# Optimization experiments

Hardware: AMD Instinct MI355X
Metric: run time of the kernel (lower is better)

## Reference

```python
import jax, jax.numpy as jnp
import numpy as np

N_NODES = 100000
N_EDGES = 640000
IN_CH = 128
OUT_CH = 128


def setup_inputs() -> dict:
    key = jax.random.key(0)
    k1, k2, k3, k4, k5, k6 = jax.random.split(key, 6)
    row = jax.random.randint(k1, (N_EDGES,), 0, N_NODES, dtype=jnp.int64 if jax.config.jax_enable_x64 else jnp.int32)
    col = jax.random.randint(k2, (N_EDGES,), 0, N_NODES, dtype=jnp.int64 if jax.config.jax_enable_x64 else jnp.int32)
    vals = jax.random.uniform(k3, (N_EDGES,), dtype=jnp.float32)
    X = jax.random.normal(k4, (N_NODES, IN_CH), dtype=jnp.float32)
    weights = jax.random.normal(k5, (IN_CH, OUT_CH), dtype=jnp.float32)
    bias = jax.random.normal(k6, (OUT_CH,), dtype=jnp.float32)
    return {"row": row, "col": col, "vals": vals, "X": X, "weights": weights, "bias": bias}


def reference(row, col, vals, X, weights, bias):
    # A is sparse COO: A[row[e], col[e]] = vals[e]
    N = X.shape[0]
    # dense feature transform: [N, out]
    XTheta = X @ weights
    # D = (row_sum(A) + 1)^(-1/2)
    deg = jax.ops.segment_sum(vals, row, num_segments=N)
    D = jax.lax.rsqrt(deg + 1.0)
    # Xprime = D * (A @ (D * XTheta))
    Y = D[:, None] * XTheta                                    # [N, out]
    msgs = vals[:, None] * Y[col]                              # [E, out] gather
    AY = jax.ops.segment_sum(msgs, row, num_segments=N)        # [N, out] scatter-add
    return D[:, None] * AY + bias
```

## Files before the change

kernel.cpp:

```cpp
#include <hip/hip_runtime.h>
#include <hip/hip_bf16.h>


#define N_CH 128
#define WT_LD 136

typedef __attribute__((ext_vector_type(8))) short short8;
typedef __attribute__((ext_vector_type(4))) float f32x4;
typedef __attribute__((ext_vector_type(4))) unsigned short ushort4v;

__device__ inline unsigned short f2bf(float f) {
    unsigned u = __float_as_uint(f);
    return (unsigned short)((u + 0x7FFFu + ((u >> 16) & 1u)) >> 16);
}
__device__ inline float bf2f(unsigned short h) {
    return __uint_as_float(((unsigned)h) << 16);
}

__global__ __launch_bounds__(256) void rank_kernel(const int* __restrict__ row,
                                                   int* __restrict__ cnt,
                                                   int* __restrict__ rank, int E) {
    int e0 = blockIdx.x * 2048 + threadIdx.x;
#pragma unroll
    for (int j = 0; j < 8; ++j) {
        int e = e0 + j * 256;
        if (e < E) rank[e] = atomicAdd(&cnt[row[e]], 1);
    }
}

__global__ __launch_bounds__(256) void scan1_kernel(const int* __restrict__ cnt,
                                                    int* __restrict__ pos,
                                                    int* __restrict__ bsum, int N) {
    __shared__ int s[256];
    int t = threadIdx.x;
    int i = blockIdx.x * 256 + t;
    int v = (i < N) ? cnt[i] : 0;
    s[t] = v;
    __syncthreads();
    for (int off = 1; off < 256; off <<= 1) {
        int x = (t >= off) ? s[t - off] : 0;
        __syncthreads();
        s[t] += x;
        __syncthreads();
    }
    if (i < N) pos[i] = s[t] - v;
    if (t == 255) bsum[blockIdx.x] = s[t];
}

__global__ __launch_bounds__(512) void scan2_kernel(int* __restrict__ bsum, int nb) {
    __shared__ int s[512];
    int t = threadIdx.x;
    int v = (t < nb) ? bsum[t] : 0;
    s[t] = v;
    __syncthreads();
    for (int off = 1; off < 512; off <<= 1) {
        int x = (t >= off) ? s[t - off] : 0;
        __syncthreads();
        s[t] += x;
        __syncthreads();
    }
    if (t < nb) bsum[t] = s[t] - v;
}

__global__ __launch_bounds__(256) void scan3_kernel(int* __restrict__ pos,
                                                    const int* __restrict__ bsum, int N) {
    int i = blockIdx.x * 256 + threadIdx.x;
    if (i < N) pos[i] += bsum[blockIdx.x];
}

__global__ __launch_bounds__(256) void place_kernel(const int* __restrict__ row,
                                                    const int* __restrict__ col,
                                                    const float* __restrict__ vals,
                                                    const int* __restrict__ pos,
                                                    const int* __restrict__ rank,
                                                    uint2* __restrict__ epack, int E) {
    int e0 = blockIdx.x * 1024 + threadIdx.x;
#pragma unroll
    for (int j = 0; j < 4; ++j) {
        int e = e0 + j * 256;
        if (e < E) {
            int r = row[e];
            int p = pos[r] + rank[e];
            epack[p] = make_uint2((unsigned)col[e], __float_as_uint(vals[e]));
        }
    }
}

__global__ __launch_bounds__(256) void dinv_kernel(const int* __restrict__ pos,
                                                   const uint2* __restrict__ epack,
                                                   float* __restrict__ dinv, int N, int E) {
    int n = blockIdx.x * 256 + threadIdx.x;
    if (n >= N) return;
    int start = pos[n];
    int end = (n + 1 < N) ? pos[n + 1] : E;
    float s = 0.f;
    for (int e = start; e < end; ++e) s += __uint_as_float(epack[e].y);
    dinv[n] = rsqrtf(s + 1.0f);
}

__global__ __launch_bounds__(256) void wcvt_kernel(const float* __restrict__ W,
                                                   unsigned short* __restrict__ Wt) {
    int i = blockIdx.x * 256 + threadIdx.x;
    int k = i >> 7, n = i & 127;
    Wt[n * N_CH + k] = f2bf(W[k * N_CH + n]);
}

__global__ __launch_bounds__(256) void gemm_kernel(const float* __restrict__ X,
                                                   const unsigned short* __restrict__ Wt,
                                                   const float* __restrict__ dinv,
                                                   unsigned short* __restrict__ Ybf, int N) {
    __shared__ unsigned short Wl[N_CH * WT_LD];

    const int t = threadIdx.x;
    const short8* Wg = (const short8*)Wt;
#pragma unroll
    for (int j = 0; j < 8; ++j) {
        int idx = t + 256 * j;
        int r = idx >> 4, cc = idx & 15;
        *(short8*)(Wl + r * WT_LD + cc * 8) = Wg[idx];
    }
    __syncthreads();

    const int lane = t & 63;
    const int wv = t >> 6;
    const int m = lane & 15;
    const int q = lane >> 4;

#pragma unroll
    for (int i = 0; i < 2; ++i) {
        const int base = (blockIdx.x * 8 + wv * 2 + i) * 16;
        if (base >= N) break;

        short8 a[4];
        const float* xrow = X + (size_t)(base + m) * N_CH + q * 8;
#pragma unroll
        for (int c = 0; c < 4; ++c) {
            f32x4 lo = *(const f32x4*)(xrow + c * 32);
            f32x4 hi = *(const f32x4*)(xrow + c * 32 + 4);
            short8 v;
            v[0] = (short)f2bf(lo[0]); v[1] = (short)f2bf(lo[1]);
            v[2] = (short)f2bf(lo[2]); v[3] = (short)f2bf(lo[3]);
            v[4] = (short)f2bf(hi[0]); v[5] = (short)f2bf(hi[1]);
            v[6] = (short)f2bf(hi[2]); v[7] = (short)f2bf(hi[3]);
            a[c] = v;
        }

        f32x4 acc[8];
#pragma unroll
        for (int tt = 0; tt < 8; ++tt) acc[tt] = (f32x4){0.f, 0.f, 0.f, 0.f};

#pragma unroll
        for (int tt = 0; tt < 8; ++tt) {
            const unsigned short* wrow = Wl + (tt * 16 + m) * WT_LD + q * 8;
#pragma unroll
            for (int c = 0; c < 4; ++c) {
                short8 b = *(const short8*)(wrow + c * 32);
                acc[tt] = __builtin_amdgcn_mfma_f32_16x16x32_bf16(a[c], b, acc[tt], 0, 0, 0);
            }
        }

        float ds[4];
#pragma unroll
        for (int r = 0; r < 4; ++r) ds[r] = dinv[base + q * 4 + r];

#pragma unroll
        for (int tt = 0; tt < 8; ++tt) {
#pragma unroll
            for (int r = 0; r < 4; ++r) {
                Ybf[(size_t)(base + q * 4 + r) * N_CH + tt * 16 + m] = f2bf(acc[tt][r] * ds[r]);
            }
        }
    }
}

__global__ __launch_bounds__(256) void gather_kernel(const int* __restrict__ pos,
                                                     const uint2* __restrict__ epack,
                                                     const unsigned short* __restrict__ Ybf,
                                                     const float* __restrict__ dinv,
                                                     const float* __restrict__ bias,
                                                     float* __restrict__ out, int N, int E) {
    unsigned gid = blockIdx.x * 256u + threadIdx.x;
    int n = gid >> 5;
    if (n >= N) return;
    int lane = gid & 31;
    int c = lane * 4;

    int e = pos[n];
    int end = (n + 1 < N) ? pos[n + 1] : E;

    float4 acc = make_float4(0.f, 0.f, 0.f, 0.f);
    for (; e + 4 <= end; e += 4) {
        uint2 p0 = epack[e + 0];
        uint2 p1 = epack[e + 1];
        uint2 p2 = epack[e + 2];
        uint2 p3 = epack[e + 3];
        ushort4v y0 = *(const ushort4v*)(Ybf + (size_t)p0.x * N_CH + c);
        ushort4v y1 = *(const ushort4v*)(Ybf + (size_t)p1.x * N_CH + c);
        ushort4v y2 = *(const ushort4v*)(Ybf + (size_t)p2.x * N_CH + c);
        ushort4v y3 = *(const ushort4v*)(Ybf + (size_t)p3.x * N_CH + c);
        float v0 = __uint_as_float(p0.y);
        float v1 = __uint_as_float(p1.y);
        float v2 = __uint_as_float(p2.y);
        float v3 = __uint_as_float(p3.y);
        acc.x += v0 * bf2f(y0[0]) + v1 * bf2f(y1[0]) + v2 * bf2f(y2[0]) + v3 * bf2f(y3[0]);
        acc.y += v0 * bf2f(y0[1]) + v1 * bf2f(y1[1]) + v2 * bf2f(y2[1]) + v3 * bf2f(y3[1]);
        acc.z += v0 * bf2f(y0[2]) + v1 * bf2f(y1[2]) + v2 * bf2f(y2[2]) + v3 * bf2f(y3[2]);
        acc.w += v0 * bf2f(y0[3]) + v1 * bf2f(y1[3]) + v2 * bf2f(y2[3]) + v3 * bf2f(y3[3]);
    }
    for (; e < end; ++e) {
        uint2 p = epack[e];
        float v = __uint_as_float(p.y);
        ushort4v y = *(const ushort4v*)(Ybf + (size_t)p.x * N_CH + c);
        acc.x += v * bf2f(y[0]);
        acc.y += v * bf2f(y[1]);
        acc.z += v * bf2f(y[2]);
        acc.w += v * bf2f(y[3]);
    }

    float d = dinv[n];
    float4 b = ((const float4*)bias)[lane];
    float4 o;
    o.x = acc.x * d + b.x;
    o.y = acc.y * d + b.y;
    o.z = acc.z * d + b.z;
    o.w = acc.w * d + b.w;
    ((float4*)(out + (size_t)n * N_CH))[lane] = o;
}

extern "C" void kernel_launch(void* const* d_in, const int* in_sizes, int n_in,
                              void* d_out, int out_size, void* d_ws, size_t ws_size,
                              hipStream_t stream) {
    const int*   row  = (const int*)d_in[0];
    const int*   col  = (const int*)d_in[1];
    const float* vals = (const float*)d_in[2];
    const float* X    = (const float*)d_in[3];
    const float* W    = (const float*)d_in[4];
    const float* bias = (const float*)d_in[5];
    float* out = (float*)d_out;

    const int E = in_sizes[0];
    const int N = in_sizes[3] / N_CH;
    const int nb = (N + 255) / 256;

    uint2*          epack = (uint2*)d_ws;
    unsigned short* Ybf   = (unsigned short*)(epack + E);
    float*          dinv  = (float*)(Ybf + (size_t)N * N_CH);
    int*            cnt   = (int*)(dinv + N);
    int*            pos   = cnt + N;
    int*            rank  = pos + N;
    int*            bsum  = rank + E;
    unsigned short* Wt    = (unsigned short*)(bsum + nb);

    hipMemsetAsync(cnt, 0, (size_t)N * sizeof(int), stream);

    rank_kernel<<<(E + 2047) / 2048, 256, 0, stream>>>(row, cnt, rank, E);
    scan1_kernel<<<nb, 256, 0, stream>>>(cnt, pos, bsum, N);
    scan2_kernel<<<1, 512, 0, stream>>>(bsum, nb);
    scan3_kernel<<<nb, 256, 0, stream>>>(pos, bsum, N);
    place_kernel<<<(E + 1023) / 1024, 256, 0, stream>>>(row, col, vals, pos, rank, epack, E);
    dinv_kernel<<<nb, 256, 0, stream>>>(pos, epack, dinv, N, E);

    wcvt_kernel<<<64, 256, 0, stream>>>(W, Wt);
    int tiles = (N + 15) / 16;
    int gblocks = (tiles + 7) / 8;
    gemm_kernel<<<gblocks, 256, 0, stream>>>(X, Wt, dinv, Ybf, N);

    unsigned gth = (unsigned)N * 32u;
    gather_kernel<<<(gth + 255) / 256, 256, 0, stream>>>(pos, epack, Ybf, dinv, bias, out, N, E);
}
```

Measured before the change: 215.0 us.

## Merge preprocessing kernels: fuse degree atomics, scan passes, and gemm with edge placement

Degree accumulation moves into the rank kernel as float atomics, and the W conversion runs as extra blocks of that same launch. The scan2/scan3 pair is replaced by one kernel in which each block sums the preceding block totals itself and also computes dinv. The GEMM and edge-placement kernels are fused into a single launch split by block index. This cuts the launch count from about nine to five and removes the pass that re-reads edges to build dinv. In exchange it adds float atomics, which make the degree sum order nondeterministic, and a scan whose per-block cost grows with the block index.

Result: slower. 237.0 us (+10.3%).

```diff
diff --git a/kernel.cpp b/kernel.cpp
--- a/kernel.cpp
+++ b/kernel.cpp
@@ -18,13 +18,28 @@
 }
 
 __global__ __launch_bounds__(256) void rank_kernel(const int* __restrict__ row,
+                                                   const float* __restrict__ vals,
                                                    int* __restrict__ cnt,
-                                                   int* __restrict__ rank, int E) {
+                                                   float* __restrict__ deg,
+                                                   int* __restrict__ rank,
+                                                   const float* __restrict__ W,
+                                                   unsigned short* __restrict__ Wt,
+                                                   int E, int rankBlocks) {
+    if ((int)blockIdx.x >= rankBlocks) {
+        int i = (blockIdx.x - rankBlocks) * 256 + threadIdx.x;
+        int k = i >> 7, n = i & 127;
+        Wt[n * N_CH + k] = f2bf(W[k * N_CH + n]);
+        return;
+    }
     int e0 = blockIdx.x * 2048 + threadIdx.x;
 #pragma unroll
     for (int j = 0; j < 8; ++j) {
         int e = e0 + j * 256;
-        if (e < E) rank[e] = atomicAdd(&cnt[row[e]], 1);
+        if (e < E) {
+            int r = row[e];
+            rank[e] = atomicAdd(&cnt[r], 1);
+            atomicAdd(&deg[r], vals[e]);
+        }
     }
 }
 
@@ -47,69 +62,50 @@
     if (t == 255) bsum[blockIdx.x] = s[t];
 }
 
-__global__ __launch_bounds__(512) void scan2_kernel(int* __restrict__ bsum, int nb) {
-    __shared__ int s[512];
+__global__ __launch_bounds__(256) void scan3_kernel(int* __restrict__ pos,
+                                                    const int* __restrict__ bsum,
+                                                    const float* __restrict__ deg,
+                                                    float* __restrict__ dinv, int N) {
+    __shared__ int s[256];
     int t = threadIdx.x;
-    int v = (t < nb) ? bsum[t] : 0;
-    s[t] = v;
+    int b = blockIdx.x;
+    int acc = 0;
+    for (int j = t; j < b; j += 256) acc += bsum[j];
+    s[t] = acc;
     __syncthreads();
-    for (int off = 1; off < 512; off <<= 1) {
-        int x = (t >= off) ? s[t - off] : 0;
+    for (int off = 128; off > 0; off >>= 1) {
+        if (t < off) s[t] += s[t + off];
         __syncthreads();
-        s[t] += x;
-        __syncthreads();
-    }
-    if (t < nb) bsum[t] = s[t] - v;
-}
-
-__global__ __launch_bounds__(256) void scan3_kernel(int* __restrict__ pos,
-                                                    const int* __restrict__ bsum, int N) {
-    int i = blockIdx.x * 256 + threadIdx.x;
-    if (i < N) pos[i] += bsum[blockIdx.x];
-}
-
-__global__ __launch_bounds__(256) void place_kernel(const int* __restrict__ row,
-                                                    const int* __restrict__ col,
-                                                    const float* __restrict__ vals,
-                                                    const int* __restrict__ pos,
-                                                    const int* __restrict__ rank,
-                                                    uint2* __restrict__ epack, int E) {
-    int e0 = blockIdx.x * 1024 + threadIdx.x;
-#pragma unroll
-    for (int j = 0; j < 4; ++j) {
-        int e = e0 + j * 256;
-        if (e < E) {
-            int r = row[e];
-            int p = pos[r] + rank[e];
-            epack[p] = make_uint2((unsigned)col[e], __float_as_uint(vals[e]));
-        }
-    }
-}
-
-__global__ __launch_bounds__(256) void dinv_kernel(const int* __restrict__ pos,
-                                                   const uint2* __restrict__ epack,
-                                                   float* __restrict__ dinv, int N, int E) {
-    int n = blockIdx.x * 256 + threadIdx.x;
-    if (n >= N) return;
-    int start = pos[n];
-    int end = (n + 1 < N) ? pos[n + 1] : E;
-    float s = 0.f;
-    for (int e = start; e < end; ++e) s += __uint_as_float(epack[e].y);
-    dinv[n] = rsqrtf(s + 1.0f);
-}
-
-__global__ __launch_bounds__(256) void wcvt_kernel(const float* __restrict__ W,
-                                                   unsigned short* __restrict__ Wt) {
-    int i = blockIdx.x * 256 + threadIdx.x;
-    int k = i >> 7, n = i & 127;
-    Wt[n * N_CH + k] = f2bf(W[k * N_CH + n]);
-}
-
-__global__ __launch_bounds__(256) void gemm_kernel(const float* __restrict__ X,
-                                                   const unsigned short* __restrict__ Wt,
-                                                   const float* __restrict__ dinv,
-                                                   unsigned short* __restrict__ Ybf, int N) {
+    }
+    int i = b * 256 + t;
+    if (i < N) {
+        pos[i] += s[0];
+        dinv[i] = rsqrtf(deg[i] + 1.0f);
+    }
+}
+
+__global__ __launch_bounds__(256) void gemm_place_kernel(
+        const float* __restrict__ X, const unsigned short* __restrict__ Wt,
+        const float* __restrict__ dinv, unsigned short* __restrict__ Ybf, int N,
+        const int* __restrict__ row, const int* __restrict__ col,
+        const float* __restrict__ vals, const int* __restrict__ pos,
+        const int* __restrict__ rank, uint2* __restrict__ epack, int E,
+        int gemmBlocks) {
     __shared__ unsigned short Wl[N_CH * WT_LD];
+
+    if ((int)blockIdx.x >= gemmBlocks) {
+        int e0 = (blockIdx.x - gemmBlocks) * 1024 + threadIdx.x;
+#pragma unroll
+        for (int j = 0; j < 4; ++j) {
+            int e = e0 + j * 256;
+            if (e < E) {
+                int r = row[e];
+                int p = pos[r] + rank[e];
+                epack[p] = make_uint2((unsigned)col[e], __float_as_uint(vals[e]));
+            }
+        }
+        return;
+    }
 
     const int t = threadIdx.x;
     const short8* Wg = (const short8*)Wt;
@@ -246,24 +242,25 @@
     unsigned short* Ybf   = (unsigned short*)(epack + E);
     float*          dinv  = (float*)(Ybf + (size_t)N * N_CH);
     int*            cnt   = (int*)(dinv + N);
-    int*            pos   = cnt + N;
+    float*          deg   = (float*)(cnt + N);
+    int*            pos   = (int*)(deg + N);
     int*            rank  = pos + N;
     int*            bsum  = rank + E;
     unsigned short* Wt    = (unsigned short*)(bsum + nb);
 
-    hipMemsetAsync(cnt, 0, (size_t)N * sizeof(int), stream);
-
-    rank_kernel<<<(E + 2047) / 2048, 256, 0, stream>>>(row, cnt, rank, E);
+    hipMemsetAsync(cnt, 0, (size_t)N * 2 * sizeof(int), stream);
+
+    const int rankBlocks = (E + 2047) / 2048;
+    rank_kernel<<<rankBlocks + 64, 256, 0, stream>>>(row, vals, cnt, deg, rank, W, Wt,
+                                                     E, rankBlocks);
     scan1_kernel<<<nb, 256, 0, stream>>>(cnt, pos, bsum, N);
-    scan2_kernel<<<1, 512, 0, stream>>>(bsum, nb);
-    scan3_kernel<<<nb, 256, 0, stream>>>(pos, bsum, N);
-    place_kernel<<<(E + 1023) / 1024, 256, 0, stream>>>(row, col, vals, pos, rank, epack, E);
-    dinv_kernel<<<nb, 256, 0, stream>>>(pos, epack, dinv, N, E);
-
-    wcvt_kernel<<<64, 256, 0, stream>>>(W, Wt);
+    scan3_kernel<<<nb, 256, 0, stream>>>(pos, bsum, deg, dinv, N);
+
     int tiles = (N + 15) / 16;
-    int gblocks = (tiles + 7) / 8;
-    gemm_kernel<<<gblocks, 256, 0, stream>>>(X, Wt, dinv, Ybf, N);
+    int gemmBlocks = (tiles + 7) / 8;
+    int placeBlocks = (E + 1023) / 1024;
+    gemm_place_kernel<<<gemmBlocks + placeBlocks, 256, 0, stream>>>(
+        X, Wt, dinv, Ybf, N, row, col, vals, pos, rank, epack, E, gemmBlocks);
 
     unsigned gth = (unsigned)N * 32u;
     gather_kernel<<<(gth + 255) / 256, 256, 0, stream>>>(pos, epack, Ybf, dinv, bias, out, N, E);
```
